# Optimization experiments

Measured on AMD Instinct MI355X. Metric: run time of the kernel, lower is better.

The kernel has to match this reference:

```python
import jax, jax.numpy as jnp
import numpy as np
from jax.scipy.special import logsumexp


def _mixture_log_cdf(x, pi, mu, s):
    # x: [B,C,H,W]; pi,mu,s: [B,C,H,W,K]. log CDF of mixture of logistics.
    z = (x[..., None] - mu) * jnp.exp(-s)
    return logsumexp(jax.nn.log_softmax(pi, axis=-1) + jax.nn.log_sigmoid(z), axis=-1)


def _mixture_log_pdf(x, pi, mu, s):
    z = (x[..., None] - mu) * jnp.exp(-s)
    log_p = z - s - 2.0 * jax.nn.softplus(z)  # logistic log-density per component
    return logsumexp(jax.nn.log_softmax(pi, axis=-1) + log_p, axis=-1)


def setup_inputs() -> dict:
    key = jax.random.key(0)
    ks = jax.random.split(key, 8)
    B, C, H, W, K = 32, 8, 64, 64, 16
    shp = (B, C, H, W)
    mshp = (B, C, H, W, K)
    return {
        "x_change": jax.random.normal(ks[0], shp, jnp.float32),
        "x_id": jax.random.normal(ks[1], shp, jnp.float32),
        "sldj": jnp.zeros((B,), jnp.float32),
        "a": 0.1 * jax.random.normal(ks[2], shp, jnp.float32),
        "b": 0.1 * jax.random.normal(ks[3], shp, jnp.float32),
        "pi": jax.random.normal(ks[4], mshp, jnp.float32),
        "mu": jax.random.normal(ks[5], mshp, jnp.float32),
        "s": 0.1 * jax.random.normal(ks[6], mshp, jnp.float32),
    }


def reference(x_change, x_id, sldj, a, b, pi, mu, s):
    B = x_change.shape[0]
    # forward (reverse=False) Flow++ MixLogCDF coupling
    log_cdf = _mixture_log_cdf(x_change, pi, mu, s)  # [B,C,H,W], values <= 0
    u = jnp.exp(log_cdf)                             # CDF in (0,1)
    # sigmoid inverse (logit) with log-det: z = log(u) - log(1-u); ldj = -log(u) - log(1-u)
    out = log_cdf - jnp.log1p(-u)
    scale_ldj = -log_cdf - jnp.log1p(-u)
    out = (out + b) * jnp.exp(a)
    logistic_ldj = _mixture_log_pdf(x_change, pi, mu, s)
    sldj = sldj + jnp.sum((logistic_ldj + scale_ldj + a).reshape(B, -1), axis=-1)
    return out, x_id, sldj
```

## Files before the change

kernel.cpp:

```cpp
#include <hip/hip_runtime.h>
#include <math.h>

#define NELEM 1048576
#define CHW 32768
#define TILE 256
#define NBLK (NELEM / TILE)
#define LOG2E 1.44269504088896340736f
#define LN2   0.69314718055994530942f

typedef const __attribute__((address_space(1))) void g_void;
typedef __attribute__((address_space(3))) void l_void;

__global__ void init_sldj_kernel(const float* __restrict__ sldj,
                                 float* __restrict__ out_sldj, int B) {
    int i = blockIdx.x * blockDim.x + threadIdx.x;
    if (i < B) out_sldj[i] = sldj[i];
}

__global__ __launch_bounds__(256) void coupling_kernel(
    const float* __restrict__ x_change, const float* __restrict__ x_id,
    const float* __restrict__ a, const float* __restrict__ b,
    const float* __restrict__ pi, const float* __restrict__ mu,
    const float* __restrict__ s, float* __restrict__ out) {
    __shared__ __align__(16) float ldsP[TILE * 16];
    __shared__ __align__(16) float ldsM[TILE * 16];
    __shared__ __align__(16) float ldsS[TILE * 16];

    const int t = threadIdx.x;
    const int w = t >> 6;
    const int l = t & 63;
    const int e0 = blockIdx.x * TILE;

    {
        const size_t gbase = (size_t)e0 * 16 + (size_t)(w * 1024 + l * 4);
        const int lbase = w * 1024 + l * 4;
#pragma unroll
        for (int c = 0; c < 4; ++c) {
            __builtin_amdgcn_global_load_lds((g_void*)(pi + gbase + c * 256),
                                             (l_void*)(ldsP + lbase + c * 256), 16, 0, 0);
            __builtin_amdgcn_global_load_lds((g_void*)(mu + gbase + c * 256),
                                             (l_void*)(ldsM + lbase + c * 256), 16, 0, 0);
            __builtin_amdgcn_global_load_lds((g_void*)(s + gbase + c * 256),
                                             (l_void*)(ldsS + lbase + c * 256), 16, 0, 0);
        }
    }

    const int kq = t & 3;
    const int g = t >> 2;
    float xv[4], av[4], bv[4];
#pragma unroll
    for (int p = 0; p < 4; ++p) {
        const int e = e0 + p * 64 + g;
        xv[p] = x_change[e];
        av[p] = a[e];
        bv[p] = b[e];
    }
    out[(size_t)NELEM + e0 + t] = x_id[e0 + t];

    __builtin_amdgcn_s_waitcnt(0);
    __syncthreads();

    float ldj = 0.0f;
    const float4* P4 = (const float4*)ldsP;
    const float4* M4 = (const float4*)ldsM;
    const float4* S4 = (const float4*)ldsS;
#pragma unroll
    for (int p = 0; p < 4; ++p) {
        const int idx = (p * 64 + g) * 4 + kq;
        const float4 pv = P4[idx];
        const float4 mv = M4[idx];
        const float4 sv = S4[idx];
        const float x = xv[p];

        float psum = 0.0f, cdf = 0.0f, omu = 0.0f, pdf = 0.0f;
        const float pk[4] = {pv.x, pv.y, pv.z, pv.w};
        const float mk[4] = {mv.x, mv.y, mv.z, mv.w};
        const float sk[4] = {sv.x, sv.y, sv.z, sv.w};
#pragma unroll
        for (int j = 0; j < 4; ++j) {
            const float wk = __builtin_amdgcn_exp2f(pk[j] * LOG2E);
            const float ez = __builtin_amdgcn_exp2f(-sk[j] * LOG2E);
            const float z = (x - mk[j]) * ez;
            const float enz = __builtin_amdgcn_exp2f(-z * LOG2E);
            const float gg = __builtin_amdgcn_rcpf(1.0f + enz);
            const float wg = wk * gg;
            psum += wk;
            cdf += wg;
            omu += wg * enz;
            pdf += wk * ez * gg * gg * enz;
        }
        psum += __shfl_xor(psum, 1); psum += __shfl_xor(psum, 2);
        cdf  += __shfl_xor(cdf, 1);  cdf  += __shfl_xor(cdf, 2);
        omu  += __shfl_xor(omu, 1);  omu  += __shfl_xor(omu, 2);
        pdf  += __shfl_xor(pdf, 1);  pdf  += __shfl_xor(pdf, 2);

        if (kq == 0) {
            const float l2psum = __builtin_amdgcn_logf(psum);
            const float l2cdf  = __builtin_amdgcn_logf(cdf);
            const float l2omu  = __builtin_amdgcn_logf(fmaxf(omu, 1e-38f));
            const float l2pdf  = __builtin_amdgcn_logf(fmaxf(pdf, 1e-38f));
            const float outv = (l2cdf - l2omu) * LN2;
            out[e0 + p * 64 + g] = (outv + bv[p]) * __builtin_amdgcn_exp2f(av[p] * LOG2E);
            ldj += (l2pdf + l2psum - l2cdf - l2omu) * LN2 + av[p];
        }
    }

    float v = ldj;
#pragma unroll
    for (int off = 32; off > 0; off >>= 1) v += __shfl_down(v, off);
    __shared__ float ws[4];
    if ((t & 63) == 0) ws[w] = v;
    __syncthreads();
    if (t == 0) {
        const float tot = ws[0] + ws[1] + ws[2] + ws[3];
        const int batch = blockIdx.x >> 7;
        atomicAdd(out + 2 * (size_t)NELEM + batch, tot);
    }
}

extern "C" void kernel_launch(void* const* d_in, const int* in_sizes, int n_in,
                              void* d_out, int out_size, void* d_ws, size_t ws_size,
                              hipStream_t stream) {
    const float* x_change = (const float*)d_in[0];
    const float* x_id     = (const float*)d_in[1];
    const float* sldj     = (const float*)d_in[2];
    const float* a        = (const float*)d_in[3];
    const float* b        = (const float*)d_in[4];
    const float* pi       = (const float*)d_in[5];
    const float* mu       = (const float*)d_in[6];
    const float* s        = (const float*)d_in[7];
    float* out = (float*)d_out;

    const int B = in_sizes[2];

    init_sldj_kernel<<<1, 64, 0, stream>>>(sldj, out + 2 * (size_t)NELEM, B);
    coupling_kernel<<<NBLK, 256, 0, stream>>>(x_change, x_id, a, b, pi, mu, s, out);
}
```

Measured before the change: 231.1 us.

## Replace LDS staging with register-prefetched persistent loop over 8 element tiles

The global_load_lds staging of pi/mu/s into shared memory is replaced by direct float4 register loads. Each block now loops over 8 groups of 64 elements and prefetches the next group's operands while computing the current one. The grid shrinks to 2048 blocks, which cuts atomics per batch, and occupancy is hinted via launch bounds. The init kernel is replaced by hipMemcpyAsync. Memory-level parallelism now depends on the software prefetch rather than many resident blocks, so latency hiding could suffer.

```diff
diff --git a/kernel.cpp b/kernel.cpp
--- a/kernel.cpp
+++ b/kernel.cpp
@@ -2,92 +2,59 @@
 #include <math.h>
 
 #define NELEM 1048576
-#define CHW 32768
-#define TILE 256
-#define NBLK (NELEM / TILE)
+#define NBLK 2048
+#define ITERS 8
 #define LOG2E 1.44269504088896340736f
 #define LN2   0.69314718055994530942f
 
-typedef const __attribute__((address_space(1))) void g_void;
-typedef __attribute__((address_space(3))) void l_void;
-
-__global__ void init_sldj_kernel(const float* __restrict__ sldj,
-                                 float* __restrict__ out_sldj, int B) {
-    int i = blockIdx.x * blockDim.x + threadIdx.x;
-    if (i < B) out_sldj[i] = sldj[i];
-}
-
-__global__ __launch_bounds__(256) void coupling_kernel(
+__global__ __launch_bounds__(256, 7) void coupling_kernel(
     const float* __restrict__ x_change, const float* __restrict__ x_id,
     const float* __restrict__ a, const float* __restrict__ b,
-    const float* __restrict__ pi, const float* __restrict__ mu,
-    const float* __restrict__ s, float* __restrict__ out) {
-    __shared__ __align__(16) float ldsP[TILE * 16];
-    __shared__ __align__(16) float ldsM[TILE * 16];
-    __shared__ __align__(16) float ldsS[TILE * 16];
+    const float4* __restrict__ pi4, const float4* __restrict__ mu4,
+    const float4* __restrict__ s4, float* __restrict__ out) {
+    const int t = threadIdx.x;
+    const int kq = t & 3;
+    const int g = t >> 2;
+    const int e0 = blockIdx.x * (64 * ITERS);
 
-    const int t = threadIdx.x;
-    const int w = t >> 6;
-    const int l = t & 63;
-    const int e0 = blockIdx.x * TILE;
-
-    {
-        const size_t gbase = (size_t)e0 * 16 + (size_t)(w * 1024 + l * 4);
-        const int lbase = w * 1024 + l * 4;
-#pragma unroll
-        for (int c = 0; c < 4; ++c) {
-            __builtin_amdgcn_global_load_lds((g_void*)(pi + gbase + c * 256),
-                                             (l_void*)(ldsP + lbase + c * 256), 16, 0, 0);
-            __builtin_amdgcn_global_load_lds((g_void*)(mu + gbase + c * 256),
-                                             (l_void*)(ldsM + lbase + c * 256), 16, 0, 0);
-            __builtin_amdgcn_global_load_lds((g_void*)(s + gbase + c * 256),
-                                             (l_void*)(ldsS + lbase + c * 256), 16, 0, 0);
-        }
+    if (t < 128) {
+        ((float4*)(out + NELEM + e0))[t] = ((const float4*)(x_id + e0))[t];
     }
 
-    const int kq = t & 3;
-    const int g = t >> 2;
-    float xv[4], av[4], bv[4];
-#pragma unroll
-    for (int p = 0; p < 4; ++p) {
-        const int e = e0 + p * 64 + g;
-        xv[p] = x_change[e];
-        av[p] = a[e];
-        bv[p] = b[e];
-    }
-    out[(size_t)NELEM + e0 + t] = x_id[e0 + t];
-
-    __builtin_amdgcn_s_waitcnt(0);
-    __syncthreads();
+    int e = e0 + g;
+    float4 P = pi4[(size_t)e * 4 + kq];
+    float4 M = mu4[(size_t)e * 4 + kq];
+    float4 S = s4[(size_t)e * 4 + kq];
+    float x = x_change[e], av = a[e], bv = b[e];
 
     float ldj = 0.0f;
-    const float4* P4 = (const float4*)ldsP;
-    const float4* M4 = (const float4*)ldsM;
-    const float4* S4 = (const float4*)ldsS;
-#pragma unroll
-    for (int p = 0; p < 4; ++p) {
-        const int idx = (p * 64 + g) * 4 + kq;
-        const float4 pv = P4[idx];
-        const float4 mv = M4[idx];
-        const float4 sv = S4[idx];
-        const float x = xv[p];
+
+#pragma unroll 2
+    for (int it = 0; it < ITERS; ++it) {
+        const int en = (it + 1 < ITERS) ? (e + 64) : e;
+        const float4 Pn = pi4[(size_t)en * 4 + kq];
+        const float4 Mn = mu4[(size_t)en * 4 + kq];
+        const float4 Sn = s4[(size_t)en * 4 + kq];
+        const float xn = x_change[en], avn = a[en], bvn = b[en];
 
         float psum = 0.0f, cdf = 0.0f, omu = 0.0f, pdf = 0.0f;
-        const float pk[4] = {pv.x, pv.y, pv.z, pv.w};
-        const float mk[4] = {mv.x, mv.y, mv.z, mv.w};
-        const float sk[4] = {sv.x, sv.y, sv.z, sv.w};
+        {
+            const float pk[4] = {P.x, P.y, P.z, P.w};
+            const float mk[4] = {M.x, M.y, M.z, M.w};
+            const float sk[4] = {S.x, S.y, S.z, S.w};
 #pragma unroll
-        for (int j = 0; j < 4; ++j) {
-            const float wk = __builtin_amdgcn_exp2f(pk[j] * LOG2E);
-            const float ez = __builtin_amdgcn_exp2f(-sk[j] * LOG2E);
-            const float z = (x - mk[j]) * ez;
-            const float enz = __builtin_amdgcn_exp2f(-z * LOG2E);
-            const float gg = __builtin_amdgcn_rcpf(1.0f + enz);
-            const float wg = wk * gg;
-            psum += wk;
-            cdf += wg;
-            omu += wg * enz;
-            pdf += wk * ez * gg * gg * enz;
+            for (int j = 0; j < 4; ++j) {
+                const float wk = __builtin_amdgcn_exp2f(pk[j] * LOG2E);
+                const float ez = __builtin_amdgcn_exp2f(-sk[j] * LOG2E);
+                const float z = (x - mk[j]) * ez;
+                const float enz = __builtin_amdgcn_exp2f(-z * LOG2E);
+                const float gg = __builtin_amdgcn_rcpf(1.0f + enz);
+                const float wg = wk * gg;
+                psum += wk;
+                cdf += wg;
+                omu += wg * enz;
+                pdf += wk * ez * gg * gg * enz;
+            }
         }
         psum += __shfl_xor(psum, 1); psum += __shfl_xor(psum, 2);
         cdf  += __shfl_xor(cdf, 1);  cdf  += __shfl_xor(cdf, 2);
@@ -99,21 +66,23 @@
             const float l2cdf  = __builtin_amdgcn_logf(cdf);
             const float l2omu  = __builtin_amdgcn_logf(fmaxf(omu, 1e-38f));
             const float l2pdf  = __builtin_amdgcn_logf(fmaxf(pdf, 1e-38f));
-            const float outv = (l2cdf - l2omu) * LN2;
-            out[e0 + p * 64 + g] = (outv + bv[p]) * __builtin_amdgcn_exp2f(av[p] * LOG2E);
-            ldj += (l2pdf + l2psum - l2cdf - l2omu) * LN2 + av[p];
+            out[e] = ((l2cdf - l2omu) * LN2 + bv) * __builtin_amdgcn_exp2f(av * LOG2E);
+            ldj += (l2pdf + l2psum - l2cdf - l2omu) * LN2 + av;
         }
+
+        P = Pn; M = Mn; S = Sn; x = xn; av = avn; bv = bvn; e = en;
     }
 
     float v = ldj;
 #pragma unroll
     for (int off = 32; off > 0; off >>= 1) v += __shfl_down(v, off);
     __shared__ float ws[4];
+    const int w = t >> 6;
     if ((t & 63) == 0) ws[w] = v;
     __syncthreads();
     if (t == 0) {
         const float tot = ws[0] + ws[1] + ws[2] + ws[3];
-        const int batch = blockIdx.x >> 7;
+        const int batch = blockIdx.x >> 6;
         atomicAdd(out + 2 * (size_t)NELEM + batch, tot);
     }
 }
@@ -126,13 +95,15 @@
     const float* sldj     = (const float*)d_in[2];
     const float* a        = (const float*)d_in[3];
     const float* b        = (const float*)d_in[4];
-    const float* pi       = (const float*)d_in[5];
-    const float* mu       = (const float*)d_in[6];
-    const float* s        = (const float*)d_in[7];
+    const float4* pi      = (const float4*)d_in[5];
+    const float4* mu      = (const float4*)d_in[6];
+    const float4* s       = (const float4*)d_in[7];
     float* out = (float*)d_out;
 
     const int B = in_sizes[2];
 
-    init_sldj_kernel<<<1, 64, 0, stream>>>(sldj, out + 2 * (size_t)NELEM, B);
+    hipMemcpyAsync(out + 2 * (size_t)NELEM, sldj, B * sizeof(float),
+                   hipMemcpyDeviceToDevice, stream);
+
     coupling_kernel<<<NBLK, 256, 0, stream>>>(x_change, x_id, a, b, pi, mu, s, out);
 }
```

After: 222.5 us. -3.7%, faster.
